# Kernel optimization log

Measured on AMD Instinct MI355X. Metric: run time of the kernel, lower is better.

The kernel has to match this reference:

```python
import jax, jax.numpy as jnp
import numpy as np

B, CIN, COUT, K, H, W, WDIM = 16, 512, 512, 3, 64, 64, 512


def setup_inputs() -> dict:
    key = jax.random.key(0)
    k1, k2, k3, k4 = jax.random.split(key, 4)
    x = jax.random.normal(k1, (B, CIN, H, W), dtype=jnp.float32)
    w = jax.random.normal(k2, (B, WDIM), dtype=jnp.float32)
    # Equalized-LR init: init_std = 1/lrmul = 1.0 -> unit normal weights
    conv_w = jax.random.normal(k3, (K, K, CIN, COUT), dtype=jnp.float32)
    mod_w = jax.random.normal(k4, (WDIM, CIN), dtype=jnp.float32)
    mod_b = jnp.zeros((CIN,), dtype=jnp.float32)
    return {"x": x, "w": w, "conv_w": conv_w, "mod_w": mod_w, "mod_b": mod_b}


def reference(x, w, conv_w, mod_w, mod_b):
    # runtime coefficients (gain=1, lrmul=1): he_std = gain/sqrt(fan_in)
    coef_conv = np.float32(1.0 / np.sqrt(K * K * CIN))
    coef_mod = np.float32(1.0 / np.sqrt(WDIM))

    # style modulation: Dense + Bias + 1.0  -> [B, CIN]
    style = w @ (coef_mod * mod_w) + mod_b + 1.0

    # per-sample modulated weight [B, K, K, CIN, COUT]
    weight = (coef_conv * conv_w)[None] * style[:, None, None, :, None]

    # demodulate: rsqrt of sum of squares over (K, K, CIN) per output channel
    d = jax.lax.rsqrt(jnp.sum(jnp.square(weight), axis=(1, 2, 3)) + 1e-8)  # [B, COUT]
    weight = weight * d[:, None, None, None, :]

    # grouped conv via batch->channel-group reshape (StyleGAN2 trick)
    wg = jnp.transpose(weight, (1, 2, 3, 0, 4)).reshape(K, K, CIN, B * COUT)
    xg = x.reshape(1, B * CIN, H, W)
    y = jax.lax.conv_general_dilated(
        xg, wg, window_strides=(1, 1), padding="SAME",
        dimension_numbers=("NCHW", "HWIO", "NCHW"),
        feature_group_count=B,
    )
    return y.reshape(B, COUT, H, W)
```

## Files before the change

kernel.cpp:

```cpp
#include <hip/hip_runtime.h>
#include <hip/hip_bf16.h>

#define NB    16
#define CIN   512
#define COUT  512
#define HH    64
#define WW    64
#define HWSZ  4096
#define WDIMN 512

typedef __attribute__((ext_vector_type(8))) short bf16x8;
typedef __attribute__((ext_vector_type(4))) float f32x4;

__device__ __forceinline__ unsigned short f2bf(float f) {
    unsigned int u = __float_as_uint(f);
    unsigned int lsb = (u >> 16) & 1u;
    u += 0x7fffu + lsb;
    return (unsigned short)(u >> 16);
}

__device__ __forceinline__ void gload_lds16(const void* g, void* l) {
    __builtin_amdgcn_global_load_lds(
        (const __attribute__((address_space(1))) unsigned char*)g,
        (__attribute__((address_space(3))) unsigned char*)l,
        16, 0, 0);
}

__global__ void k_style(const float* __restrict__ w, const float* __restrict__ mod_w,
                        const float* __restrict__ mod_b, float* __restrict__ style) {
    const int b = blockIdx.x, t = threadIdx.x;
    __shared__ float wl[WDIMN];
    wl[t] = w[b * WDIMN + t];
    wl[t + 256] = w[b * WDIMN + t + 256];
    __syncthreads();
    float a0 = 0.f, a1 = 0.f;
    const int c0 = t, c1 = t + 256;
    for (int j = 0; j < WDIMN; ++j) {
        const float wj = wl[j];
        a0 += wj * mod_w[j * CIN + c0];
        a1 += wj * mod_w[j * CIN + c1];
    }
    const float coef = 0.044194173824159216f;
    style[b * CIN + c0] = coef * a0 + mod_b[c0] + 1.0f;
    style[b * CIN + c1] = coef * a1 + mod_b[c1] + 1.0f;
}

__global__ void k_s2(const float* __restrict__ cw, float* __restrict__ s2) {
    const int i = blockIdx.x * 256 + threadIdx.x;
    float a = 0.f;
#pragma unroll
    for (int tap = 0; tap < 9; ++tap) {
        const float v = cw[tap * (CIN * COUT) + i];
        a += v * v;
    }
    s2[i] = a;
}

__global__ void k_demod(const float* __restrict__ style, const float* __restrict__ s2,
                        float* __restrict__ dd) {
    const int b = blockIdx.x, t = threadIdx.x;
    __shared__ float st2[CIN];
    {
        const float s0 = style[b * CIN + t], s1 = style[b * CIN + t + 256];
        st2[t] = s0 * s0;
        st2[t + 256] = s1 * s1;
    }
    __syncthreads();
    float a0 = 0.f, a1 = 0.f;
    for (int ci = 0; ci < CIN; ++ci) {
        const float sv = st2[ci];
        a0 += sv * s2[ci * COUT + t];
        a1 += sv * s2[ci * COUT + t + 256];
    }
    const float c2 = 1.0f / 4608.0f;
    dd[b * COUT + t] = rsqrtf(c2 * a0 + 1e-8f);
    dd[b * COUT + t + 256] = rsqrtf(c2 * a1 + 1e-8f);
}

__global__ void k_wmod(const float* __restrict__ cw, const float* __restrict__ style,
                       const float* __restrict__ dd, unsigned short* __restrict__ wmod,
                       int b_start, int gcount) {
    const int tap = blockIdx.x;
    const int co0 = blockIdx.y * 64;
    const int ci0 = blockIdx.z * 128;
    const int t = threadIdx.x;

    __shared__ float tile[128][65];
    __shared__ float sst[16 * 128];
    {
        const int j = t & 63, isub = t >> 6;
        for (int i = isub; i < 128; i += 4)
            tile[i][j] = cw[(size_t)tap * CIN * COUT + (size_t)(ci0 + i) * COUT + co0 + j];
    }
    for (int i = t; i < gcount * 128; i += 256)
        sst[i] = style[(b_start + (i >> 7)) * CIN + ci0 + (i & 127)];
    __syncthreads();

    const float coef = 0.014731391274719736f;
    const int cq = t & 31;
    const int rsub = t >> 5;
    const int totrows = gcount * 64;
    for (int g = rsub; g < totrows; g += 8) {
        const int bbl = g >> 6;
        const int co_r = g & 63;
        const int bg = b_start + bbl;
        const float dv = dd[bg * COUT + co0 + co_r] * coef;
        const float v0 = tile[4 * cq + 0][co_r] * sst[bbl * 128 + 4 * cq + 0] * dv;
        const float v1 = tile[4 * cq + 1][co_r] * sst[bbl * 128 + 4 * cq + 1] * dv;
        const float v2 = tile[4 * cq + 2][co_r] * sst[bbl * 128 + 4 * cq + 2] * dv;
        const float v3 = tile[4 * cq + 3][co_r] * sst[bbl * 128 + 4 * cq + 3] * dv;
        uint2 pk;
        pk.x = (unsigned int)f2bf(v0) | ((unsigned int)f2bf(v1) << 16);
        pk.y = (unsigned int)f2bf(v2) | ((unsigned int)f2bf(v3) << 16);
        *(uint2*)&wmod[((size_t)(bbl * 9 + tap) * COUT + co0 + co_r) * CIN + ci0 + 4 * cq] = pk;
    }
}

__global__ void k_xt(const float* __restrict__ x, unsigned short* __restrict__ xT, int b_start) {
    const int bbl = blockIdx.x;
    const int b = b_start + bbl;
    const int hw0 = blockIdx.y * 64;
    const int ci0 = blockIdx.z * 64;
    const int t = threadIdx.x;

    __shared__ float tile[64][65];
    {
        const int j = t & 63, isub = t >> 6;
        for (int i = isub; i < 64; i += 4)
            tile[i][j] = x[((size_t)b * CIN + ci0 + i) * HWSZ + hw0 + j];
    }
    __syncthreads();

    const int cq = t & 15;
    const int rs = t >> 4;
    for (int r = rs; r < 64; r += 16) {
        const float v0 = tile[4 * cq + 0][r];
        const float v1 = tile[4 * cq + 1][r];
        const float v2 = tile[4 * cq + 2][r];
        const float v3 = tile[4 * cq + 3][r];
        uint2 pk;
        pk.x = (unsigned int)f2bf(v0) | ((unsigned int)f2bf(v1) << 16);
        pk.y = (unsigned int)f2bf(v2) | ((unsigned int)f2bf(v3) << 16);
        *(uint2*)&xT[((size_t)bbl * HWSZ + hw0 + r) * CIN + ci0 + 4 * cq] = pk;
    }
}

__global__ __launch_bounds__(256, 2)
void k_conv(const unsigned short* __restrict__ xT, const unsigned short* __restrict__ wmod,
            float* __restrict__ out, int b_start, int gcount) {
    int st, ct, bbl;
    {
        const int id = blockIdx.x;
        if (gcount == 16) {
            const int xcd = id & 7;
            const int slot = id >> 3;
            bbl = xcd + 8 * (slot >> 7);
            const int rem = slot & 127;
            ct = rem >> 5;
            st = rem & 31;
        } else {
            st = id & 31; ct = (id >> 5) & 3; bbl = id >> 7;
        }
    }
    const int b = b_start + bbl;
    const int r0 = st * 2;
    const int co0 = ct * 128;

    const int t = threadIdx.x;
    const int lane = t & 63;
    const int wid = t >> 6;
    const int wrow = wid >> 1;
    const int wcol = wid & 1;

    __shared__ __align__(16) unsigned char smem[4 * 66 * 128 + 2 * 128 * 128];
    unsigned char* Xs = smem;
    unsigned char* As = smem + 4 * 66 * 128;

    const f32x4 fzero = {0.f, 0.f, 0.f, 0.f};

    if (t < 64) {
        const int s = t >> 3;
        const int row = s >> 1, col = (s & 1) ? 65 : 0;
        *(f32x4*)(Xs + (row * 66 + col) * 128 + (t & 7) * 16) = fzero;
    }
    if (r0 == 0) {
        for (int idx = t; idx < 66 * 8; idx += 256)
            *(f32x4*)(Xs + (idx >> 3) * 128 + (idx & 7) * 16) = fzero;
    }
    if (r0 == 62) {
        for (int idx = t; idx < 66 * 8; idx += 256)
            *(f32x4*)(Xs + (3 * 66 + (idx >> 3)) * 128 + (idx & 7) * 16) = fzero;
    }

    f32x4 acc[4][4];
#pragma unroll
    for (int i = 0; i < 4; ++i)
#pragma unroll
        for (int j = 0; j < 4; ++j) acc[i][j] = fzero;

    const size_t xTbase = (size_t)bbl * HWSZ * CIN;

    auto stageA = [&](int gidx) {
        const int tap2 = gidx % 9, cc2 = gidx / 9;
        const unsigned short* gb = wmod + ((size_t)(bbl * 9 + tap2) * COUT + co0) * CIN + cc2 * 64;
        unsigned char* dbase = As + (gidx & 1) * 16384;
#pragma unroll
        for (int i = 0; i < 4; ++i) {
            const int la = wid + 4 * i;
            const int row = la * 8 + (lane >> 3);
            const int kb = ((lane & 7) * 16) ^ ((row & 7) << 4);
            gload_lds16((const unsigned char*)(gb + (size_t)row * CIN) + kb,
                        dbase + la * 1024);
        }
    };
    auto stageX = [&](int ccn) {
        const int ci0 = ccn * 64;
#pragma unroll
        for (int i = 0; i < 8; ++i) {
            const int li = wid + 4 * i;
            const int row = li >> 3;
            const int c0 = 1 + (li & 7) * 8;
            const int ih = r0 - 1 + row;
            if (ih >= 0 && ih < HH) {
                const int col = c0 + (lane >> 3);
                const int pxidx = row * 66 + col;
                const int kb = ((lane & 7) * 16) ^ ((pxidx & 7) << 4);
                gload_lds16((const unsigned char*)(xT + xTbase + (size_t)(ih * WW + col - 1) * CIN + ci0) + kb,
                            Xs + (row * 66 + c0) * 128);
            }
        }
    };

    stageX(0);
    stageA(0);
    stageA(1);
    asm volatile("s_waitcnt vmcnt(4) lgkmcnt(0)" ::: "memory");
    __builtin_amdgcn_s_barrier();

    for (int cc = 0; cc < 8; ++cc) {
#pragma unroll
        for (int tap = 0; tap < 9; ++tap) {
            const int g = cc * 9 + tap;
            const unsigned char* Ab = As + (g & 1) * 16384;
            const int dh = tap / 3 - 1, dw = tap % 3 - 1;

#pragma unroll
            for (int k32 = 0; k32 < 2; ++k32) {
                bf16x8 af[4], bfv[4];
#pragma unroll
                for (int ma = 0; ma < 4; ++ma) {
                    const int co_r = wrow * 64 + ma * 16 + (lane & 15);
                    const int kb = (k32 * 64 + (lane >> 4) * 16) ^ ((co_r & 7) << 4);
                    af[ma] = *(const bf16x8*)(Ab + co_r * 128 + kb);
                }
#pragma unroll
                for (int nb = 0; nb < 4; ++nb) {
                    const int px = wcol * 64 + nb * 16 + (lane & 15);
                    const int trow = (px >> 6) + 1 + dh;
                    const int tcol = (px & 63) + 1 + dw;
                    const int pxidx = trow * 66 + tcol;
                    const int kb = (k32 * 64 + (lane >> 4) * 16) ^ ((pxidx & 7) << 4);
                    bfv[nb] = *(const bf16x8*)(Xs + pxidx * 128 + kb);
                }
#pragma unroll
                for (int ma = 0; ma < 4; ++ma)
#pragma unroll
                    for (int nb = 0; nb < 4; ++nb)
                        acc[ma][nb] = __builtin_amdgcn_mfma_f32_16x16x32_bf16(
                            af[ma], bfv[nb], acc[ma][nb], 0, 0, 0);
            }

            asm volatile("s_waitcnt lgkmcnt(0)" ::: "memory");
            __builtin_amdgcn_s_barrier();

            if (tap == 8 && cc < 7) stageX(cc + 1);
            if (g < 70) stageA(g + 2);

            if (g == 70) asm volatile("s_waitcnt vmcnt(0)" ::: "memory");
            else         asm volatile("s_waitcnt vmcnt(4)" ::: "memory");
            __builtin_amdgcn_s_barrier();
        }
    }

#pragma unroll
    for (int ma = 0; ma < 4; ++ma) {
        const int co = co0 + wrow * 64 + ma * 16 + ((lane >> 4) << 2);
#pragma unroll
        for (int nb = 0; nb < 4; ++nb) {
            const int px = wcol * 64 + nb * 16 + (lane & 15);
            const int oh = r0 + (px >> 6);
            const int ow = px & 63;
            float* o = out + (((size_t)b * COUT + co) * HH + oh) * WW + ow;
#pragma unroll
            for (int jj = 0; jj < 4; ++jj) o[(size_t)jj * HWSZ] = acc[ma][nb][jj];
        }
    }
}

extern "C" void kernel_launch(void* const* d_in, const int* in_sizes, int n_in,
                              void* d_out, int out_size, void* d_ws, size_t ws_size,
                              hipStream_t stream) {
    (void)in_sizes; (void)n_in; (void)out_size;
    const float* x     = (const float*)d_in[0];
    const float* w     = (const float*)d_in[1];
    const float* convw = (const float*)d_in[2];
    const float* mod_w = (const float*)d_in[3];
    const float* mod_b = (const float*)d_in[4];
    float* out = (float*)d_out;

    unsigned char* ws = (unsigned char*)d_ws;
    const size_t OFF_STYLE = 0;
    const size_t OFF_S2 = 32768;
    const size_t OFF_D = OFF_S2 + 1048576;
    const size_t OFF_BIG = OFF_D + 32768;
    const size_t PER_B_W = (size_t)9 * COUT * CIN * 2;
    const size_t PER_B_X = (size_t)HWSZ * CIN * 2;
    const size_t PER_B = PER_B_W + PER_B_X;

    if (ws_size < OFF_BIG + PER_B) return;
    const size_t avail = ws_size - OFF_BIG;
    const int G = (avail >= 16 * PER_B) ? 16 : (avail >= 4 * PER_B ? 4 : 1);

    float* style = (float*)(ws + OFF_STYLE);
    float* s2    = (float*)(ws + OFF_S2);
    float* dd    = (float*)(ws + OFF_D);
    unsigned short* wmod = (unsigned short*)(ws + OFF_BIG);
    unsigned short* xT   = (unsigned short*)(ws + OFF_BIG + (size_t)G * PER_B_W);

    k_style<<<dim3(16), dim3(256), 0, stream>>>(w, mod_w, mod_b, style);
    k_s2<<<dim3(1024), dim3(256), 0, stream>>>(convw, s2);
    k_demod<<<dim3(16), dim3(256), 0, stream>>>(style, s2, dd);

    for (int b0 = 0; b0 < NB; b0 += G) {
        k_wmod<<<dim3(9, 8, 4), dim3(256), 0, stream>>>(convw, style, dd, wmod, b0, G);
        k_xt<<<dim3(G, 64, 8), dim3(256), 0, stream>>>(x, xT, b0);
        k_conv<<<dim3(32 * 4 * G), dim3(256), 0, stream>>>(xT, wmod, out, b0, G);
    }
}
```

Measured before the change: 391.5 us.

## Prelayout weights as MFMA fragments, load A to registers, double-buffer X tile

Measured after the change: 595.9 us. +52.2%, slower.

```diff
diff --git a/kernel.cpp b/kernel.cpp
--- a/kernel.cpp
+++ b/kernel.cpp
@@ -112,7 +112,18 @@
         uint2 pk;
         pk.x = (unsigned int)f2bf(v0) | ((unsigned int)f2bf(v1) << 16);
         pk.y = (unsigned int)f2bf(v2) | ((unsigned int)f2bf(v3) << 16);
-        *(uint2*)&wmod[((size_t)(bbl * 9 + tap) * COUT + co0 + co_r) * CIN + ci0 + 4 * cq] = pk;
+        const int co_g = co0 + co_r;
+        const int ct4 = co_g >> 7;
+        const int rg  = (co_g >> 4) & 7;
+        const int lo  = co_g & 15;
+        const int ci_g = ci0 + 4 * cq;
+        const int cc2 = ci_g >> 6;
+        const int k32 = (ci_g >> 5) & 1;
+        const int hi  = (ci_g >> 3) & 3;
+        const int j0  = ci_g & 7;
+        const size_t eoff = ((((((size_t)(bbl * 9 + tap) * 4 + ct4) * 8 + cc2) * 2 + k32) * 8 + rg) * 64
+                             + hi * 16 + lo) * 8 + j0;
+        *(uint2*)&wmod[eoff] = pk;
     }
 }
 
@@ -145,8 +156,9 @@
     }
 }
 
+#define XBUF 33792
 __global__ __launch_bounds__(256, 2)
-void k_conv(const unsigned short* __restrict__ xT, const unsigned short* __restrict__ wmod,
+void k_conv(const unsigned short* __restrict__ xT, const unsigned short* __restrict__ afrag,
             float* __restrict__ out, int b_start, int gcount) {
     int st, ct, bbl;
     {
@@ -172,24 +184,29 @@
     const int wrow = wid >> 1;
     const int wcol = wid & 1;
 
-    __shared__ __align__(16) unsigned char smem[4 * 66 * 128 + 2 * 128 * 128];
-    unsigned char* Xs = smem;
-    unsigned char* As = smem + 4 * 66 * 128;
+    __shared__ __align__(16) unsigned char smem[2 * XBUF];
 
     const f32x4 fzero = {0.f, 0.f, 0.f, 0.f};
 
-    if (t < 64) {
+    if (t < 128) {
         const int s = t >> 3;
-        const int row = s >> 1, col = (s & 1) ? 65 : 0;
-        *(f32x4*)(Xs + (row * 66 + col) * 128 + (t & 7) * 16) = fzero;
+        unsigned char* Xb = smem + ((s >> 3) & 1) * XBUF;
+        const int row = (s >> 1) & 3, col = (s & 1) ? 65 : 0;
+        *(f32x4*)(Xb + (row * 66 + col) * 128 + (t & 7) * 16) = fzero;
     }
     if (r0 == 0) {
-        for (int idx = t; idx < 66 * 8; idx += 256)
-            *(f32x4*)(Xs + (idx >> 3) * 128 + (idx & 7) * 16) = fzero;
+        for (int idx = t; idx < 2 * 66 * 8; idx += 256) {
+            unsigned char* Xb = smem + (idx >= 66 * 8 ? XBUF : 0);
+            const int k = idx % (66 * 8);
+            *(f32x4*)(Xb + (k >> 3) * 128 + (k & 7) * 16) = fzero;
+        }
     }
     if (r0 == 62) {
-        for (int idx = t; idx < 66 * 8; idx += 256)
-            *(f32x4*)(Xs + (3 * 66 + (idx >> 3)) * 128 + (idx & 7) * 16) = fzero;
+        for (int idx = t; idx < 2 * 66 * 8; idx += 256) {
+            unsigned char* Xb = smem + (idx >= 66 * 8 ? XBUF : 0);
+            const int k = idx % (66 * 8);
+            *(f32x4*)(Xb + (3 * 66 + (k >> 3)) * 128 + (k & 7) * 16) = fzero;
+        }
     }
 
     f32x4 acc[4][4];
@@ -200,20 +217,7 @@
 
     const size_t xTbase = (size_t)bbl * HWSZ * CIN;
 
-    auto stageA = [&](int gidx) {
-        const int tap2 = gidx % 9, cc2 = gidx / 9;
-        const unsigned short* gb = wmod + ((size_t)(bbl * 9 + tap2) * COUT + co0) * CIN + cc2 * 64;
-        unsigned char* dbase = As + (gidx & 1) * 16384;
-#pragma unroll
-        for (int i = 0; i < 4; ++i) {
-            const int la = wid + 4 * i;
-            const int row = la * 8 + (lane >> 3);
-            const int kb = ((lane & 7) * 16) ^ ((row & 7) << 4);
-            gload_lds16((const unsigned char*)(gb + (size_t)row * CIN) + kb,
-                        dbase + la * 1024);
-        }
-    };
-    auto stageX = [&](int ccn) {
+    auto stageX = [&](int ccn, unsigned char* dst) {
         const int ci0 = ccn * 64;
 #pragma unroll
         for (int i = 0; i < 8; ++i) {
@@ -226,59 +230,83 @@
                 const int pxidx = row * 66 + col;
                 const int kb = ((lane & 7) * 16) ^ ((pxidx & 7) << 4);
                 gload_lds16((const unsigned char*)(xT + xTbase + (size_t)(ih * WW + col - 1) * CIN + ci0) + kb,
-                            Xs + (row * 66 + c0) * 128);
+                            dst + (row * 66 + c0) * 128);
             }
         }
     };
 
-    stageX(0);
-    stageA(0);
-    stageA(1);
-    asm volatile("s_waitcnt vmcnt(4) lgkmcnt(0)" ::: "memory");
+    auto loadA = [&](int tap2, int cc2, bf16x8 (&dst)[2][4]) {
+        const unsigned short* base = afrag
+            + (size_t)((((bbl * 9 + tap2) * 4 + ct) * 8 + cc2) * 2) * 4096
+            + (wrow * 4) * 512 + lane * 8;
+#pragma unroll
+        for (int k32 = 0; k32 < 2; ++k32)
+#pragma unroll
+            for (int ma = 0; ma < 4; ++ma)
+                dst[k32][ma] = *(const bf16x8*)(base + k32 * 4096 + ma * 512);
+    };
+
+    auto mfma_tap = [&](const unsigned char* Xcur, int dh, int dw, bf16x8 (&A)[2][4]) {
+#pragma unroll
+        for (int k32 = 0; k32 < 2; ++k32) {
+            bf16x8 bfv[4];
+#pragma unroll
+            for (int nb = 0; nb < 4; ++nb) {
+                const int px = wcol * 64 + nb * 16 + (lane & 15);
+                const int trow = (px >> 6) + 1 + dh;
+                const int tcol = (px & 63) + 1 + dw;
+                const int pxidx = trow * 66 + tcol;
+                const int kb = (k32 * 64 + (lane >> 4) * 16) ^ ((pxidx & 7) << 4);
+                bfv[nb] = *(const bf16x8*)(Xcur + pxidx * 128 + kb);
+            }
+#pragma unroll
+            for (int ma = 0; ma < 4; ++ma)
+#pragma unroll
+                for (int nb = 0; nb < 4; ++nb)
+                    acc[ma][nb] = __builtin_amdgcn_mfma_f32_16x16x32_bf16(
+                        A[k32][ma], bfv[nb], acc[ma][nb], 0, 0, 0);
+        }
+    };
+
+    bf16x8 aE[2][4], aO[2][4];
+
+    stageX(0, smem);
+    asm volatile("s_waitcnt vmcnt(0) lgkmcnt(0)" ::: "memory");
     __builtin_amdgcn_s_barrier();
-
-    for (int cc = 0; cc < 8; ++cc) {
-#pragma unroll
-        for (int tap = 0; tap < 9; ++tap) {
-            const int g = cc * 9 + tap;
-            const unsigned char* Ab = As + (g & 1) * 16384;
-            const int dh = tap / 3 - 1, dw = tap % 3 - 1;
-
-#pragma unroll
-            for (int k32 = 0; k32 < 2; ++k32) {
-                bf16x8 af[4], bfv[4];
-#pragma unroll
-                for (int ma = 0; ma < 4; ++ma) {
-                    const int co_r = wrow * 64 + ma * 16 + (lane & 15);
-                    const int kb = (k32 * 64 + (lane >> 4) * 16) ^ ((co_r & 7) << 4);
-                    af[ma] = *(const bf16x8*)(Ab + co_r * 128 + kb);
+    loadA(0, 0, aE);
+
+    for (int ccp = 0; ccp < 4; ++ccp) {
+#pragma unroll
+        for (int t18 = 0; t18 < 18; ++t18) {
+            const int h = t18 / 9;
+            const int tap9 = t18 % 9;
+            const int cc = 2 * ccp + h;
+            unsigned char* Xcur = smem + h * XBUF;
+            unsigned char* Xnxt = smem + (1 - h) * XBUF;
+            const int dh = tap9 / 3 - 1, dw = tap9 % 3 - 1;
+            const int p = (h + tap9) & 1;
+
+            if (tap9 == 0) {
+                if (h == 0 || ccp < 3) stageX(cc + 1, Xnxt);
+            }
+            {
+                const int tapn = (tap9 + 1) % 9;
+                const int ccn = cc + (tap9 == 8 ? 1 : 0);
+                if (p == 0) {
+                    if (!(t18 == 17) || ccp < 3) loadA(tapn, ccn, aO);
+                } else {
+                    if (!(t18 == 17) || ccp < 3) loadA(tapn, ccn, aE);
                 }
-#pragma unroll
-                for (int nb = 0; nb < 4; ++nb) {
-                    const int px = wcol * 64 + nb * 16 + (lane & 15);
-                    const int trow = (px >> 6) + 1 + dh;
-                    const int tcol = (px & 63) + 1 + dw;
-                    const int pxidx = trow * 66 + tcol;
-                    const int kb = (k32 * 64 + (lane >> 4) * 16) ^ ((pxidx & 7) << 4);
-                    bfv[nb] = *(const bf16x8*)(Xs + pxidx * 128 + kb);
-                }
-#pragma unroll
-                for (int ma = 0; ma < 4; ++ma)
-#pragma unroll
-                    for (int nb = 0; nb < 4; ++nb)
-                        acc[ma][nb] = __builtin_amdgcn_mfma_f32_16x16x32_bf16(
-                            af[ma], bfv[nb], acc[ma][nb], 0, 0, 0);
-            }
-
-            asm volatile("s_waitcnt lgkmcnt(0)" ::: "memory");
-            __builtin_amdgcn_s_barrier();
-
-            if (tap == 8 && cc < 7) stageX(cc + 1);
-            if (g < 70) stageA(g + 2);
-
-            if (g == 70) asm volatile("s_waitcnt vmcnt(0)" ::: "memory");
-            else         asm volatile("s_waitcnt vmcnt(4)" ::: "memory");
-            __builtin_amdgcn_s_barrier();
+            }
+            if (p == 0) mfma_tap(Xcur, dh, dw, aE);
+            else        mfma_tap(Xcur, dh, dw, aO);
+
+            if (tap9 == 8 && !(h == 1 && ccp == 3)) {
+                asm volatile("s_waitcnt lgkmcnt(0)" ::: "memory");
+                asm volatile("s_waitcnt vmcnt(8)" ::: "memory");
+                __builtin_amdgcn_s_barrier();
+                __builtin_amdgcn_sched_barrier(0);
+            }
         }
     }
 
```

## Fuse input transpose and bf16 conversion into conv kernel's X staging

Applied to the files above, without the earlier changes.

New measurement: 469.1 us. 1.2x slower.

```diff
diff --git a/kernel.cpp b/kernel.cpp
--- a/kernel.cpp
+++ b/kernel.cpp
@@ -116,37 +116,8 @@
     }
 }
 
-__global__ void k_xt(const float* __restrict__ x, unsigned short* __restrict__ xT, int b_start) {
-    const int bbl = blockIdx.x;
-    const int b = b_start + bbl;
-    const int hw0 = blockIdx.y * 64;
-    const int ci0 = blockIdx.z * 64;
-    const int t = threadIdx.x;
-
-    __shared__ float tile[64][65];
-    {
-        const int j = t & 63, isub = t >> 6;
-        for (int i = isub; i < 64; i += 4)
-            tile[i][j] = x[((size_t)b * CIN + ci0 + i) * HWSZ + hw0 + j];
-    }
-    __syncthreads();
-
-    const int cq = t & 15;
-    const int rs = t >> 4;
-    for (int r = rs; r < 64; r += 16) {
-        const float v0 = tile[4 * cq + 0][r];
-        const float v1 = tile[4 * cq + 1][r];
-        const float v2 = tile[4 * cq + 2][r];
-        const float v3 = tile[4 * cq + 3][r];
-        uint2 pk;
-        pk.x = (unsigned int)f2bf(v0) | ((unsigned int)f2bf(v1) << 16);
-        pk.y = (unsigned int)f2bf(v2) | ((unsigned int)f2bf(v3) << 16);
-        *(uint2*)&xT[((size_t)bbl * HWSZ + hw0 + r) * CIN + ci0 + 4 * cq] = pk;
-    }
-}
-
 __global__ __launch_bounds__(256, 2)
-void k_conv(const unsigned short* __restrict__ xT, const unsigned short* __restrict__ wmod,
+void k_conv(const float* __restrict__ x, const unsigned short* __restrict__ wmod,
             float* __restrict__ out, int b_start, int gcount) {
     int st, ct, bbl;
     {
@@ -198,8 +169,6 @@
 #pragma unroll
         for (int j = 0; j < 4; ++j) acc[i][j] = fzero;
 
-    const size_t xTbase = (size_t)bbl * HWSZ * CIN;
-
     auto stageA = [&](int gidx) {
         const int tap2 = gidx % 9, cc2 = gidx / 9;
         const unsigned short* gb = wmod + ((size_t)(bbl * 9 + tap2) * COUT + co0) * CIN + cc2 * 64;
@@ -213,20 +182,26 @@
                         dbase + la * 1024);
         }
     };
+
     auto stageX = [&](int ccn) {
         const int ci0 = ccn * 64;
 #pragma unroll
-        for (int i = 0; i < 8; ++i) {
-            const int li = wid + 4 * i;
-            const int row = li >> 3;
-            const int c0 = 1 + (li & 7) * 8;
+        for (int u = 0; u < 16; ++u) {
+            const int row = u & 3;
+            const int q = (u >> 2) * 4 + wid;
             const int ih = r0 - 1 + row;
             if (ih >= 0 && ih < HH) {
-                const int col = c0 + (lane >> 3);
-                const int pxidx = row * 66 + col;
-                const int kb = ((lane & 7) * 16) ^ ((pxidx & 7) << 4);
-                gload_lds16((const unsigned char*)(xT + xTbase + (size_t)(ih * WW + col - 1) * CIN + ci0) + kb,
-                            Xs + (row * 66 + c0) * 128);
+                const float* xp = x + ((size_t)(b * CIN + ci0 + 4 * q) * HH + ih) * WW + lane;
+                const float v0 = xp[0];
+                const float v1 = xp[HWSZ];
+                const float v2 = xp[2 * HWSZ];
+                const float v3 = xp[3 * HWSZ];
+                uint2 pk;
+                pk.x = (unsigned int)f2bf(v0) | ((unsigned int)f2bf(v1) << 16);
+                pk.y = (unsigned int)f2bf(v2) | ((unsigned int)f2bf(v3) << 16);
+                const int pxidx = row * 66 + 1 + lane;
+                const int off8 = (8 * q) ^ ((pxidx & 7) << 4);
+                *(uint2*)(Xs + pxidx * 128 + off8) = pk;
             }
         }
     };
@@ -278,6 +253,7 @@
 
             if (g == 70) asm volatile("s_waitcnt vmcnt(0)" ::: "memory");
             else         asm volatile("s_waitcnt vmcnt(4)" ::: "memory");
+            if (tap == 8) asm volatile("s_waitcnt lgkmcnt(0)" ::: "memory");
             __builtin_amdgcn_s_barrier();
         }
     }
@@ -314,18 +290,15 @@
     const size_t OFF_D = OFF_S2 + 1048576;
     const size_t OFF_BIG = OFF_D + 32768;
     const size_t PER_B_W = (size_t)9 * COUT * CIN * 2;
-    const size_t PER_B_X = (size_t)HWSZ * CIN * 2;
-    const size_t PER_B = PER_B_W + PER_B_X;
-
-    if (ws_size < OFF_BIG + PER_B) return;
+
+    if (ws_size < OFF_BIG + PER_B_W) return;
     const size_t avail = ws_size - OFF_BIG;
-    const int G = (avail >= 16 * PER_B) ? 16 : (avail >= 4 * PER_B ? 4 : 1);
+    const int G = (avail >= 16 * PER_B_W) ? 16 : (avail >= 4 * PER_B_W ? 4 : 1);
 
     float* style = (float*)(ws + OFF_STYLE);
     float* s2    = (float*)(ws + OFF_S2);
     float* dd    = (float*)(ws + OFF_D);
     unsigned short* wmod = (unsigned short*)(ws + OFF_BIG);
-    unsigned short* xT   = (unsigned short*)(ws + OFF_BIG + (size_t)G * PER_B_W);
 
     k_style<<<dim3(16), dim3(256), 0, stream>>>(w, mod_w, mod_b, style);
     k_s2<<<dim3(1024), dim3(256), 0, stream>>>(convw, s2);
@@ -333,7 +306,6 @@
 
     for (int b0 = 0; b0 < NB; b0 += G) {
         k_wmod<<<dim3(9, 8, 4), dim3(256), 0, stream>>>(convw, style, dd, wmod, b0, G);
-        k_xt<<<dim3(G, 64, 8), dim3(256), 0, stream>>>(x, xT, b0);
-        k_conv<<<dim3(32 * 4 * G), dim3(256), 0, stream>>>(xT, wmod, out, b0, G);
-    }
-}
+        k_conv<<<dim3(32 * 4 * G), dim3(256), 0, stream>>>(x, wmod, out, b0, G);
+    }
+}
```
